# Optimization experiments

Hardware: AMD Instinct MI355X
Metric: run time of the kernel (lower is better)

Reference implementation:

```python
import jax, jax.numpy as jnp
import numpy as np
from jax import lax

EPS = 1e-5
S_CENTROIDS = 2048
K_NEIGH = 32


def _fps(xyz, S):
    """Farthest point sampling. xyz: (B,N,3) -> idx (B,S) int32."""
    B, N, _ = xyz.shape

    def body(carry, _):
        dist, farthest = carry  # (B,N), (B,)
        centroid = jnp.take_along_axis(xyz, farthest[:, None, None], axis=1)  # (B,1,3)
        d = jnp.sum((xyz - centroid) ** 2, axis=-1)  # (B,N)
        dist = jnp.minimum(dist, d)
        nxt = jnp.argmax(dist, axis=-1).astype(jnp.int32)
        return (dist, nxt), farthest

    init = (jnp.full((B, N), 1e10, xyz.dtype), jnp.zeros((B,), jnp.int32))
    _, idx = lax.scan(body, init, None, length=S)
    return idx.T  # (B,S)


def _knn(q, p, K):
    """q: (B,S,3) queries, p: (B,N,3) points -> idx (B,S,K) of K nearest."""
    d = (jnp.sum(q * q, -1)[:, :, None] + jnp.sum(p * p, -1)[:, None, :]
         - 2.0 * jnp.einsum('bsd,bnd->bsn', q, p))  # (B,S,N) sq dists
    _, idx = lax.top_k(-d, K)
    return idx


def _mlp_layer(x, w, g, b, m, v):
    # x: (B,S,K,Cin); 1x1 conv == channel matmul, then eval-mode BN, then ReLU
    x = jnp.einsum('bskc,oc->bsko', x, w)
    x = (x - m) * (g * lax.rsqrt(v + EPS)) + b
    return jax.nn.relu(x)


def setup_inputs() -> dict:
    key = jax.random.key(0)
    ks = jax.random.split(key, 8)
    B, N, D = 4, 8192, 64
    inp = {
        'xyz': jax.random.normal(ks[0], (B, N, 3), jnp.float32),
        'points': jax.random.normal(ks[1], (B, D, N), jnp.float32),
        'w0': jax.random.normal(ks[2], (64, 67), jnp.float32) * (1.0 / np.sqrt(67)),
        'g0': jnp.ones((64,), jnp.float32), 'b0': jnp.zeros((64,), jnp.float32),
        'm0': jnp.zeros((64,), jnp.float32), 'v0': jnp.ones((64,), jnp.float32),
        'w1': jax.random.normal(ks[3], (64, 64), jnp.float32) * (1.0 / np.sqrt(64)),
        'g1': jnp.ones((64,), jnp.float32), 'b1': jnp.zeros((64,), jnp.float32),
        'm1': jnp.zeros((64,), jnp.float32), 'v1': jnp.ones((64,), jnp.float32),
        'w2': jax.random.normal(ks[4], (128, 64), jnp.float32) * (1.0 / np.sqrt(64)),
        'g2': jnp.ones((128,), jnp.float32), 'b2': jnp.zeros((128,), jnp.float32),
        'm2': jnp.zeros((128,), jnp.float32), 'v2': jnp.ones((128,), jnp.float32),
    }
    return inp


def reference(xyz, points, w0, g0, b0, m0, v0, w1, g1, b1, m1, v1,
              w2, g2, b2, m2, v2):
    B, N, _ = xyz.shape
    S, K = S_CENTROIDS, K_NEIGH

    # FPS centroids (S < N path of the module)
    fps_idx = _fps(xyz, S)                                        # (B,S)
    new_xyz = jnp.take_along_axis(xyz, fps_idx[..., None], axis=1)  # (B,S,3)

    # KNN grouping
    idx = _knn(new_xyz, xyz, K)                                   # (B,S,K)
    grouped_xyz = jnp.take_along_axis(xyz[:, None], idx[..., None], axis=2)  # (B,S,K,3)
    grouped_xyz = grouped_xyz - new_xyz[:, :, None, :]

    # gather neighbor features: points (B,D,N) -> (B,N,D) -> (B,S,K,D)
    pts = jnp.transpose(points, (0, 2, 1))
    neigh = jnp.take_along_axis(pts[:, None], idx[..., None], axis=2)
    grouped = jnp.concatenate([grouped_xyz, neigh], axis=-1)      # (B,S,K,3+D)

    x = _mlp_layer(grouped, w0, g0, b0, m0, v0)
    x = _mlp_layer(x, w1, g1, b1, m1, v1)
    x = _mlp_layer(x, w2, g2, b2, m2, v2)                         # (B,S,K,128)

    new_points = jnp.transpose(jnp.max(x, axis=2), (0, 2, 1))     # (B,128,S)
    return new_xyz, new_points
```

## Files before the change

kernel.cpp:

```cpp
#include <hip/hip_runtime.h>
#include <cfloat>
#include <climits>

#define NPTS   8192
#define SCENT  2048
#define KNEIGH 32
#define BATCH  4
#define DFEAT  64
#define FPS_T  512
#define NV     8
#define NW     8
#define CAP    64
#define NCONS  252
#define CPB    63

typedef float v2f __attribute__((ext_vector_type(2)));

#define DPPTOP2(um, us, ctrl, rmask)                                                  \
    { unsigned _tm = (unsigned)__builtin_amdgcn_update_dpp(0, (int)(um), (ctrl),      \
                                                           (rmask), 0xf, false);     \
      unsigned _ts = (unsigned)__builtin_amdgcn_update_dpp(0, (int)(us), (ctrl),      \
                                                           (rmask), 0xf, false);     \
      unsigned _lo = ((um) < _tm) ? (um) : _tm;                                       \
      (us) = ((us) > _ts) ? (us) : _ts;                                               \
      (us) = ((us) > _lo) ? (us) : _lo;                                               \
      (um) = ((um) > _tm) ? (um) : _tm; }

#define FLUSH_PUB(Eidx, VX, VY, VZ, HASPREV, PX, PY, PZ)                              \
    if (((Eidx) & 63) == 63) {                                                        \
        const int base0 = (Eidx) - 63;                                                \
        if (t < 64 * 3) {                                                             \
            const int ci = base0 + t / 3;                                             \
            const int cc = t - (t / 3) * 3;                                           \
            float v;                                                                  \
            if (ci == (Eidx))                                                         \
                v = (cc == 0) ? (VX) : ((cc == 1) ? (VY) : (VZ));                     \
            else if ((HASPREV) && ci == (Eidx) - 1)                                   \
                v = (cc == 0) ? (PX) : ((cc == 1) ? (PY) : (PZ));                     \
            else                                                                      \
                v = (cc == 0) ? S.hx[ci] : ((cc == 1) ? S.hy[ci] : S.hz[ci]);         \
            __hip_atomic_store(&new_xyz[((size_t)b * SCENT + base0) * 3 + t], v,      \
                               __ATOMIC_RELAXED, __HIP_MEMORY_SCOPE_AGENT);           \
        }                                                                             \
        __syncthreads();                 \
        if (t == 0)                                                                   \
            __hip_atomic_store(&progress[b], (Eidx) + 1,                              \
                               __ATOMIC_RELEASE, __HIP_MEMORY_SCOPE_AGENT);           \
    }

struct FpsSh {
    float sx[NPTS], sy[NPTS], sz[NPTS];
    float hx[SCENT], hy[SCENT], hz[SCENT];
    alignas(16) unsigned slotQ[2][NW][4];
    int scand[CAP];
    int scnt;
    alignas(8) double sdd[2][NW];
    double sfv[NW];
    int sfo[NW];
};
struct ConsSh {
    float  spx[2048], spy[2048], spz[2048];
    double sp2[2048];
    float  tile[32 * 33];
    float  regA[64 * 68];
    float  regB[64 * 64];
    float  regC[128 * 64];
    float  prm[512];
};
union ShU { FpsSh f; ConsSh c; };

__global__ __launch_bounds__(FPS_T, 1) void fused_kernel(
        const float* __restrict__ xyz, float* __restrict__ new_xyz,
        const float* __restrict__ pts, float* __restrict__ ptsT,
        int* __restrict__ progress, int* __restrict__ tcount,
        float* __restrict__ out_points,
        const float* __restrict__ w0, const float* __restrict__ g0,
        const float* __restrict__ b0, const float* __restrict__ m0,
        const float* __restrict__ v0, const float* __restrict__ w1,
        const float* __restrict__ g1, const float* __restrict__ b1,
        const float* __restrict__ m1, const float* __restrict__ v1,
        const float* __restrict__ w2, const float* __restrict__ g2,
        const float* __restrict__ b2, const float* __restrict__ m2,
        const float* __restrict__ v2) {
    __shared__ ShU sh;
    const int t = threadIdx.x;
    const int lane = t & 63, w = t >> 6;

    if (blockIdx.x < BATCH) {
        FpsSh& S = sh.f;
        const int b = blockIdx.x;
        const float* X = xyz + (size_t)b * NPTS * 3;

        for (int p = t; p < NPTS; p += FPS_T) {
            S.sx[p] = X[3 * p + 0]; S.sy[p] = X[3 * p + 1]; S.sz[p] = X[3 * p + 2];
        }

        v2f px2[NV], py2[NV], pz2[NV], dist2[NV];
#pragma unroll
        for (int j = 0; j < NV; ++j) {
            int pA = t + FPS_T * j, pB = t + FPS_T * (j + NV);
            px2[j] = (v2f){X[3 * pA + 0], X[3 * pB + 0]};
            py2[j] = (v2f){X[3 * pA + 1], X[3 * pB + 1]};
            pz2[j] = (v2f){X[3 * pA + 2], X[3 * pB + 2]};
            dist2[j] = (v2f){1e10f, 1e10f};
        }
        float c0x = X[0], c0y = X[1], c0z = X[2];
        float c1x = 0.f, c1y = 0.f, c1z = 0.f;
        int dual = 0, buf = 0;
        int E = 1;
        if (t == 0) { S.hx[0] = c0x; S.hy[0] = c0y; S.hz[0] = c0z; }
        __syncthreads();

#pragma unroll 1
        while (true) {
            float m2s = -1.f, s2s = -1.f;
            {
                const v2f cxx = {c0x, c0x}, cyy = {c0y, c0y}, czz = {c0z, c0z};
                if (dual) {
                    const v2f exx = {c1x, c1x}, eyy = {c1y, c1y}, ezz = {c1z, c1z};
#pragma unroll
                    for (int j = 0; j < NV; ++j) {
                        v2f dx = px2[j] - cxx, dy = py2[j] - cyy, dz = pz2[j] - czz;
                        v2f d0 = __builtin_elementwise_fma(dx, dx,
                                 __builtin_elementwise_fma(dy, dy, dz * dz));
                        v2f ex = px2[j] - exx, ey = py2[j] - eyy, ez = pz2[j] - ezz;
                        v2f d1 = __builtin_elementwise_fma(ex, ex,
                                 __builtin_elementwise_fma(ey, ey, ez * ez));
                        v2f d  = __builtin_elementwise_min(d0, d1);
                        v2f nd = __builtin_elementwise_min(dist2[j], d);
                        dist2[j] = nd;
                        float hi = fmaxf(nd.x, nd.y), lo = fminf(nd.x, nd.y);
                        s2s = fmaxf(fmaxf(s2s, lo), fminf(m2s, hi));
                        m2s = fmaxf(m2s, hi);
                    }
                } else {
#pragma unroll
                    for (int j = 0; j < NV; ++j) {
                        v2f dx = px2[j] - cxx, dy = py2[j] - cyy, dz = pz2[j] - czz;
                        v2f d  = __builtin_elementwise_fma(dx, dx,
                                 __builtin_elementwise_fma(dy, dy, dz * dz));
                        v2f nd = __builtin_elementwise_min(dist2[j], d);
                        dist2[j] = nd;
                        float hi = fmaxf(nd.x, nd.y), lo = fminf(nd.x, nd.y);
                        s2s = fmaxf(fmaxf(s2s, lo), fminf(m2s, hi));
                        m2s = fmaxf(m2s, hi);
                    }
                }
            }
            const float m = m2s, sec = s2s;

            int mi = 0;
#pragma unroll
            for (int j = 0; j < NV; ++j) {
                mi = (dist2[j].x == m) ? (t + FPS_T * j)        : mi;
                mi = (dist2[j].y == m) ? (t + FPS_T * (j + NV)) : mi;
            }

            const unsigned myU = __float_as_uint(m);
            unsigned um = myU, us = __float_as_uint(sec);
            DPPTOP2(um, us, 0x111, 0xf);
            DPPTOP2(um, us, 0x112, 0xf);
            DPPTOP2(um, us, 0x114, 0xf);
            DPPTOP2(um, us, 0x118, 0xf);
            DPPTOP2(um, us, 0x142, 0xa);
            DPPTOP2(um, us, 0x143, 0xc);
            const unsigned wu  = (unsigned)__builtin_amdgcn_readlane((int)um, 63);
            const unsigned wsu = (unsigned)__builtin_amdgcn_readlane((int)us, 63);

            unsigned long long wb = __ballot(myU == wu);
            const int wl   = __ffsll(wb) - 1;
            const int widx = __builtin_amdgcn_readlane(mi, wl);
            const float thwf = __fmul_rn(__uint_as_float(wu), 0.999998f);
            unsigned long long b1m = __ballot(m >= thwf);
            unsigned long long b2m = __ballot(sec >= thwf);
            const unsigned tw = (b2m || __popcll(b1m) >= 2) ? 1u : 0u;
            if (lane == 0) {
                *(uint4*)&S.slotQ[buf][w][0] =
                    make_uint4(wu, (unsigned)widx | (tw << 14), wsu, 0u);
            }
            __syncthreads();

            unsigned mv[NW], mt4[NW], sv2[NW];
            {
                const uint4* qp = (const uint4*)&S.slotQ[buf][0][0];
                uint4 u0 = qp[0], u1 = qp[1], u2 = qp[2], u3 = qp[3];
                uint4 u4 = qp[4], u5 = qp[5], u6 = qp[6], u7 = qp[7];
                mv[0]=u0.x; mt4[0]=u0.y; sv2[0]=u0.z;
                mv[1]=u1.x; mt4[1]=u1.y; sv2[1]=u1.z;
                mv[2]=u2.x; mt4[2]=u2.y; sv2[2]=u2.z;
                mv[3]=u3.x; mt4[3]=u3.y; sv2[3]=u3.z;
                mv[4]=u4.x; mt4[4]=u4.y; sv2[4]=u4.z;
                mv[5]=u5.x; mt4[5]=u5.y; sv2[5]=u5.z;
                mv[6]=u6.x; mt4[6]=u6.y; sv2[6]=u6.z;
                mv[7]=u7.x; mt4[7]=u7.y; sv2[7]=u7.z;
            }
            unsigned gu = mv[0];
#pragma unroll
            for (int k = 1; k < NW; ++k) gu = (mv[k] > gu) ? mv[k] : gu;
            const float gvf  = __uint_as_float(gu);
            const float gthf = __fmul_rn(gvf, 0.999998f);
            const unsigned ugth = __float_as_uint(gthf);
            int nw = 0; unsigned meta = 0; int kw = 0;
#pragma unroll
            for (int k = NW - 1; k >= 0; --k) {
                nw  += (mv[k] >= ugth) ? 1 : 0;
                meta = (mv[k] == gu) ? mt4[k] : meta;
                kw   = (mv[k] == gu) ? k : kw;
            }
            const int wtie = (meta >> 14) & 1;
            int i1 = (int)(meta & 0x3fffu);
            const int fb = (nw >= 2) || wtie;

            if (fb) {
                if (t == 0) S.scnt = 0;
                __syncthreads();
#pragma unroll
                for (int j = 0; j < NV; ++j) {
                    if (dist2[j].x >= gthf) {
                        int slot = atomicAdd(&S.scnt, 1);
                        if (slot < CAP) S.scand[slot] = t + FPS_T * j;
                    }
                    if (dist2[j].y >= gthf) {
                        int slot = atomicAdd(&S.scnt, 1);
                        if (slot < CAP) S.scand[slot] = t + FPS_T * (j + NV);
                    }
                }
                __syncthreads();
                const int mm = S.scnt;
                if (mm <= CAP) {
                    double bd = -1.0; int bi = INT_MAX;
#pragma unroll 1
                    for (int k = 0; k < mm; ++k) {
                        const int pos = S.scand[k];
                        const double pxd = (double)S.sx[pos], pyd = (double)S.sy[pos],
                                     pzd = (double)S.sz[pos];
                        double dd = 1e10;
                        for (int i = t; i < E; i += FPS_T) {
                            double ddx = __dsub_rn(pxd, (double)S.hx[i]);
                            double ddy = __dsub_rn(pyd, (double)S.hy[i]);
                            double ddz = __dsub_rn(pzd, (double)S.hz[i]);
                            double d = __dadd_rn(__dadd_rn(__dmul_rn(ddx, ddx), __dmul_rn(ddy, ddy)),
                                                 __dmul_rn(ddz, ddz));
                            dd = fmin(dd, d);
                        }
#pragma unroll
                        for (int off = 32; off >= 1; off >>= 1)
                            dd = fmin(dd, __shfl_down(dd, off));
                        if (lane == 0) S.sdd[k & 1][w] = dd;
                        __syncthreads();
                        double ddm = S.sdd[k & 1][0];
#pragma unroll
                        for (int w2i = 1; w2i < NW; ++w2i) ddm = fmin(ddm, S.sdd[k & 1][w2i]);
                        if (ddm > bd || (ddm == bd && pos < bi)) { bd = ddm; bi = pos; }
                    }
                    i1 = bi;
                } else {
                    double bv = -1.0; int bi = INT_MAX;
#pragma unroll 1
                    for (int j = 0; j < 2 * NV; ++j) {
                        const int jj = j & (NV - 1);
                        const bool hiHalf = j >= NV;
                        const double pxd = (double)(hiHalf ? px2[jj].y : px2[jj].x);
                        const double pyd = (double)(hiHalf ? py2[jj].y : py2[jj].x);
                        const double pzd = (double)(hiHalf ? pz2[jj].y : pz2[jj].x);
                        double dd = 1e10;
                        for (int i = 0; i < E; ++i) {
                            double ddx = __dsub_rn(pxd, (double)S.hx[i]);
                            double ddy = __dsub_rn(pyd, (double)S.hy[i]);
                            double ddz = __dsub_rn(pzd, (double)S.hz[i]);
                            double d = __dadd_rn(__dadd_rn(__dmul_rn(ddx, ddx), __dmul_rn(ddy, ddy)),
                                                 __dmul_rn(ddz, ddz));
                            dd = fmin(dd, d);
                        }
                        int pidx = t + FPS_T * j;
                        if (dd > bv || (dd == bv && pidx < bi)) { bv = dd; bi = pidx; }
                    }
#pragma unroll
                    for (int off = 32; off >= 1; off >>= 1) {
                        double ov = __shfl_down(bv, off);
                        int    oi = __shfl_down(bi, off);
                        if (ov > bv || (ov == bv && oi < bi)) { bv = ov; bi = oi; }
                    }
                    if (lane == 0) { S.sfv[w] = bv; S.sfo[w] = bi; }
                    __syncthreads();
                    bv = S.sfv[0]; bi = S.sfo[0];
#pragma unroll
                    for (int w2i = 1; w2i < NW; ++w2i) {
                        double ov = S.sfv[w2i]; int oi = S.sfo[w2i];
                        if (ov > bv || (ov == bv && oi < bi)) { bv = ov; bi = oi; }
                    }
                    i1 = bi;
                }
                __syncthreads();
            }

            const float e0x = S.sx[i1], e0y = S.sy[i1], e0z = S.sz[i1];
            if (t == 0) { S.hx[E] = e0x; S.hy[E] = e0y; S.hz[E] = e0z; }
            FLUSH_PUB(E, e0x, e0y, e0z, 0, 0.f, 0.f, 0.f);
            c0x = e0x; c0y = e0y; c0z = e0z;

            int peeled = 0;
            float e1x = 0.f, e1y = 0.f, e1z = 0.f;
            if (!fb && (E + 1) < SCENT) {
                unsigned arr[NW];
#pragma unroll
                for (int k = 0; k < NW; ++k) arr[k] = (k == kw) ? sv2[k] : mv[k];
                unsigned v2u = arr[0];
#pragma unroll
                for (int k = 1; k < NW; ++k) v2u = (arr[k] > v2u) ? arr[k] : v2u;
                int k2 = 0; unsigned meta2 = 0;
#pragma unroll
                for (int k = NW - 1; k >= 0; --k) {
                    meta2 = (arr[k] == v2u) ? mt4[k] : meta2;
                    k2    = (arr[k] == v2u) ? k : k2;
                }
                unsigned v3u = 0;
#pragma unroll
                for (int k = 0; k < NW; ++k) {
                    const unsigned cnd = (k == kw || k == k2) ? sv2[k] : mv[k];
                    v3u = (cnd > v3u) ? cnd : v3u;
                }
                const float v2vf = __uint_as_float(v2u);
                const float v3vf = __uint_as_float(v3u);
                const int i2 = (int)(meta2 & 0x3fffu);
                e1x = S.sx[i2]; e1y = S.sy[i2]; e1z = S.sz[i2];
                const float ddx = e1x - e0x, ddy = e1y - e0y, ddz = e1z - e0z;
                const float dq = fmaf(ddx, ddx, fmaf(ddy, ddy, ddz * ddz));
                const float wnew = fminf(v2vf, dq);
                peeled = ((k2 != kw) &&
                          (wnew > __fmul_rn(v3vf, 1.000004f))) ? 1 : 0;
            }
            if (peeled) {
                const int e1i = E + 1;
                if (t == 0) { S.hx[e1i] = e1x; S.hy[e1i] = e1y; S.hz[e1i] = e1z; }
                FLUSH_PUB(e1i, e1x, e1y, e1z, 1, e0x, e0y, e0z);
                c1x = e1x; c1y = e1y; c1z = e1z;
                dual = 1;
                E = e1i + 1;
            } else {
                dual = 0;
                E = E + 1;
            }
            if (E >= SCENT) break;
            buf ^= 1;
        }
    } else {
        ConsSh& K = sh.c;
        const int local = blockIdx.x - BATCH;
        const int batch = local / CPB;
        const int cl    = local % CPB;
        const int tx = t & 31, ty = t >> 5;

        for (int tid2 = local; tid2 < 2048; tid2 += NCONS) {
            const int bt = tid2 >> 9, rest = tid2 & 511;
            const int d0 = (rest >> 8) * 32, n0 = (rest & 255) * 32;
            __syncthreads();
#pragma unroll
            for (int i = 0; i < 2; ++i)
                K.tile[(ty + 16 * i) * 33 + tx] =
                    pts[(size_t)bt * DFEAT * NPTS + (size_t)(d0 + ty + 16 * i) * NPTS + n0 + tx];
            __syncthreads();
#pragma unroll
            for (int i = 0; i < 2; ++i)
                ptsT[(size_t)bt * NPTS * DFEAT + (size_t)(n0 + ty + 16 * i) * DFEAT + d0 + tx] =
                    K.tile[tx * 33 + ty + 16 * i];
        }
        if (t == 0) {
            __threadfence();
            atomicAdd(tcount, 1);
        }

        for (int idx = t; idx < 64 * 68; idx += FPS_T) {
            int o = idx / 68, i = idx - o * 68;
            float v;
            if (i < 64)      v = w0[o * 67 + 3 + i];
            else if (i < 67) v = w0[o * 67 + (i - 64)];
            else             v = 0.0f;
            K.regA[idx] = v;
        }
        for (int idx = t; idx < 64 * 64; idx += FPS_T)  K.regB[idx] = w1[idx];
        for (int idx = t; idx < 128 * 64; idx += FPS_T) K.regC[idx] = w2[idx];
        if (t < 64) {
            float a0v = g0[t] / sqrtf(v0[t] + 1e-5f);
            K.prm[t]       = a0v;
            K.prm[64 + t]  = b0[t] - m0[t] * a0v;
            float a1v = g1[t] / sqrtf(v1[t] + 1e-5f);
            K.prm[128 + t] = a1v;
            K.prm[192 + t] = b1[t] - m1[t] * a1v;
        } else if (t < 192) {
            int o = t - 64;
            float a2v = g2[o] / sqrtf(v2[o] + 1e-5f);
            K.prm[256 + o] = a2v;
            K.prm[384 + o] = b2[o] - m2[o] * a2v;
        }

        const float* Xb = xyz + (size_t)batch * NPTS * 3;
#pragma unroll 1
        for (int r = 0; ; ++r) {
            const int sBase = r * (CPB * NW) + cl * NW;
            if (sBase >= SCENT) break;
            const int sMax = min(sBase + NW - 1, SCENT - 1);
            if (t == 0) {
                while (__hip_atomic_load(&progress[batch], __ATOMIC_ACQUIRE,
                                         __HIP_MEMORY_SCOPE_AGENT) < sMax + 1)
                    __builtin_amdgcn_s_sleep(8);
                if (r == 0) {
                    while (__hip_atomic_load(tcount, __ATOMIC_ACQUIRE,
                                             __HIP_MEMORY_SCOPE_AGENT) < NCONS)
                        __builtin_amdgcn_s_sleep(8);
                }
            }
            __syncthreads();

            const int sQ = min(sBase + w, SCENT - 1);
            const float* q = new_xyz + ((size_t)batch * SCENT + sQ) * 3;
            const float qfx = q[0], qfy = q[1], qfz = q[2];
            const double qx = (double)qfx, qy = (double)qfy, qz = (double)qfz;
            const double q2 = __dadd_rn(__dadd_rn(__dmul_rn(qx, qx), __dmul_rn(qy, qy)),
                                        __dmul_rn(qz, qz));

            double ld   = DBL_MAX;
            int    li   = 0x7fffffff;
            double taud = DBL_MAX;
            int    taui = 0x7fffffff;

#pragma unroll 1
            for (int c = 0; c < 4; ++c) {
                __syncthreads();
#pragma unroll
                for (int r2 = 0; r2 < 4; ++r2) {
                    int pl = r2 * 512 + t;
                    int p  = c * 2048 + pl;
                    float x = Xb[3 * p + 0], y = Xb[3 * p + 1], z = Xb[3 * p + 2];
                    K.spx[pl] = x; K.spy[pl] = y; K.spz[pl] = z;
                    double dx = (double)x, dy = (double)y, dz = (double)z;
                    K.sp2[pl] = __dadd_rn(__dadd_rn(__dmul_rn(dx, dx), __dmul_rn(dy, dy)),
                                          __dmul_rn(dz, dz));
                }
                __syncthreads();
#pragma unroll 1
                for (int i = 0; i < 32; ++i) {
                    const int pl   = i * 64 + lane;
                    const int pidx = c * 2048 + pl;
                    double px = (double)K.spx[pl], py = (double)K.spy[pl],
                           pz = (double)K.spz[pl];
                    double qp = __dadd_rn(__dadd_rn(__dmul_rn(qx, px), __dmul_rn(qy, py)),
                                          __dmul_rn(qz, pz));
                    double d  = __dsub_rn(__dadd_rn(q2, K.sp2[pl]), __dmul_rn(2.0, qp));
                    bool cand = (d < taud) || (d == taud && pidx < taui);
                    unsigned long long mmask = __ballot(cand);
                    while (mmask) {
                        int sl = __ffsll((unsigned long long)mmask) - 1;
                        mmask &= mmask - 1;
                        double dv = __shfl(d, sl);
                        int    iv = __shfl(pidx, sl);
                        if (dv < taud || (dv == taud && iv < taui)) {
                            bool gt = (lane < 32) && (ld > dv || (ld == dv && li > iv));
                            unsigned long long gm = __ballot(gt);
                            double ud = __shfl_up(ld, 1);
                            int    ui = __shfl_up(li, 1);
                            if (gt) { ld = ud; li = ui; }
                            bool first = gt && ((lane == 0) || !((gm >> (lane - 1)) & 1ull));
                            if (first) { ld = dv; li = iv; }
                            taud = __shfl(ld, 31);
                            taui = __shfl(li, 31);
                        }
                    }
                }
            }

            if (sBase + w < SCENT && lane < 32) {
                const int nidx = li;
                const float* P3 = Xb + (size_t)nidx * 3;
                const float dx = P3[0] - qfx, dy = P3[1] - qfy, dz = P3[2] - qfz;

                const float4* F = (const float4*)(ptsT + ((size_t)batch * NPTS + nidx) * 64);
                float4 xv[17];
#pragma unroll
                for (int i = 0; i < 16; ++i) xv[i] = F[i];
                xv[16] = make_float4(dx, dy, dz, 0.0f);

                float h0[64];
                const float4* W0 = (const float4*)K.regA;
#pragma unroll
                for (int o = 0; o < 64; ++o) {
                    float acc = 0.f;
#pragma unroll
                    for (int i = 0; i < 17; ++i) {
                        float4 ww = W0[o * 17 + i];
                        acc = fmaf(xv[i].x, ww.x, acc);
                        acc = fmaf(xv[i].y, ww.y, acc);
                        acc = fmaf(xv[i].z, ww.z, acc);
                        acc = fmaf(xv[i].w, ww.w, acc);
                    }
                    h0[o] = fmaxf(fmaf(acc, K.prm[o], K.prm[64 + o]), 0.f);
                }
                float h1[64];
                const float4* W1 = (const float4*)K.regB;
#pragma unroll
                for (int o = 0; o < 64; ++o) {
                    float acc = 0.f;
#pragma unroll
                    for (int i = 0; i < 16; ++i) {
                        float4 ww = W1[o * 16 + i];
                        acc = fmaf(h0[4 * i + 0], ww.x, acc);
                        acc = fmaf(h0[4 * i + 1], ww.y, acc);
                        acc = fmaf(h0[4 * i + 2], ww.z, acc);
                        acc = fmaf(h0[4 * i + 3], ww.w, acc);
                    }
                    h1[o] = fmaxf(fmaf(acc, K.prm[128 + o], K.prm[192 + o]), 0.f);
                }
                const float4* W2 = (const float4*)K.regC;
                float* outp = out_points + (size_t)batch * 128 * SCENT + sQ;
#pragma unroll 1
                for (int o = 0; o < 128; ++o) {
                    float acc = 0.f;
#pragma unroll
                    for (int i = 0; i < 16; ++i) {
                        float4 ww = W2[o * 16 + i];
                        acc = fmaf(h1[4 * i + 0], ww.x, acc);
                        acc = fmaf(h1[4 * i + 1], ww.y, acc);
                        acc = fmaf(h1[4 * i + 2], ww.z, acc);
                        acc = fmaf(h1[4 * i + 3], ww.w, acc);
                    }
                    float y = fmaxf(fmaf(acc, K.prm[256 + o], K.prm[384 + o]), 0.f);
#pragma unroll
                    for (int off = 16; off >= 1; off >>= 1)
                        y = fmaxf(y, __shfl_xor(y, off));
                    if (lane == 0) outp[(size_t)o * SCENT] = y;
                }
            }
        }
    }
}

extern "C" void kernel_launch(void* const* d_in, const int* in_sizes, int n_in,
                              void* d_out, int out_size, void* d_ws, size_t ws_size,
                              hipStream_t stream) {
    const float* xyz    = (const float*)d_in[0];
    const float* points = (const float*)d_in[1];
    const float* w0 = (const float*)d_in[2];
    const float* g0 = (const float*)d_in[3];
    const float* b0 = (const float*)d_in[4];
    const float* m0 = (const float*)d_in[5];
    const float* v0 = (const float*)d_in[6];
    const float* w1 = (const float*)d_in[7];
    const float* g1 = (const float*)d_in[8];
    const float* b1 = (const float*)d_in[9];
    const float* m1 = (const float*)d_in[10];
    const float* v1 = (const float*)d_in[11];
    const float* w2 = (const float*)d_in[12];
    const float* g2 = (const float*)d_in[13];
    const float* b2 = (const float*)d_in[14];
    const float* m2 = (const float*)d_in[15];
    const float* v2 = (const float*)d_in[16];

    float* out_xyz    = (float*)d_out;
    float* out_points = (float*)d_out + (size_t)BATCH * SCENT * 3;

    char* ws = (char*)d_ws;
    int*   progress = (int*)ws;
    int*   tcount   = (int*)(ws + 64);
    float* ptsT     = (float*)(ws + 32768);

    hipMemsetAsync(ws, 0, 128, stream);

    void* kargs[] = { (void*)&xyz, (void*)&out_xyz, (void*)&points, (void*)&ptsT,
                      (void*)&progress, (void*)&tcount, (void*)&out_points,
                      (void*)&w0, (void*)&g0, (void*)&b0, (void*)&m0, (void*)&v0,
                      (void*)&w1, (void*)&g1, (void*)&b1, (void*)&m1, (void*)&v1,
                      (void*)&w2, (void*)&g2, (void*)&b2, (void*)&m2, (void*)&v2 };
    hipLaunchCooperativeKernel((const void*)fused_kernel,
                               dim3(BATCH + NCONS), dim3(FPS_T), kargs, 0, stream);
}
```

Before: 2.237 ms.

## Publish winner coordinates in per-wave slots and vectorize top-2 tracking in FPS

Each wave now writes the coordinates of its local max point into shared memory next to its max/second-max record. After the barrier, lanes read those slots and use readlane to get the chosen centroid's coordinates, instead of doing a dependent LDS lookup of sx/sy/sz after the index is resolved. Top-2 tracking in the distance loop is kept per vector lane and reduced once at the end. The tie flag is now derived from the wave-reduced second value rather than two ballots. This aims to shorten the serial critical path of each FPS iteration, in exchange for an extra LDS gather per lane and a wider slot array. The tie detection rule is slightly changed, which could affect the fallback decision.

```diff
diff --git a/kernel.cpp b/kernel.cpp
--- a/kernel.cpp
+++ b/kernel.cpp
@@ -51,7 +51,7 @@
 struct FpsSh {
     float sx[NPTS], sy[NPTS], sz[NPTS];
     float hx[SCENT], hy[SCENT], hz[SCENT];
-    alignas(16) unsigned slotQ[2][NW][4];
+    alignas(16) unsigned slotQ[2][NW][8];
     int scand[CAP];
     int scnt;
     alignas(8) double sdd[2][NW];
@@ -113,7 +113,7 @@
 
 #pragma unroll 1
         while (true) {
-            float m2s = -1.f, s2s = -1.f;
+            v2f m2v = {-1.f, -1.f}, s2v = {-1.f, -1.f};
             {
                 const v2f cxx = {c0x, c0x}, cyy = {c0y, c0y}, czz = {c0z, c0z};
                 if (dual) {
@@ -129,9 +129,9 @@
                         v2f d  = __builtin_elementwise_min(d0, d1);
                         v2f nd = __builtin_elementwise_min(dist2[j], d);
                         dist2[j] = nd;
-                        float hi = fmaxf(nd.x, nd.y), lo = fminf(nd.x, nd.y);
-                        s2s = fmaxf(fmaxf(s2s, lo), fminf(m2s, hi));
-                        m2s = fmaxf(m2s, hi);
+                        v2f lo = __builtin_elementwise_min(m2v, nd);
+                        s2v = __builtin_elementwise_max(s2v, lo);
+                        m2v = __builtin_elementwise_max(m2v, nd);
                     }
                 } else {
 #pragma unroll
@@ -141,13 +141,14 @@
                                  __builtin_elementwise_fma(dy, dy, dz * dz));
                         v2f nd = __builtin_elementwise_min(dist2[j], d);
                         dist2[j] = nd;
-                        float hi = fmaxf(nd.x, nd.y), lo = fminf(nd.x, nd.y);
-                        s2s = fmaxf(fmaxf(s2s, lo), fminf(m2s, hi));
-                        m2s = fmaxf(m2s, hi);
-                    }
-                }
-            }
-            const float m = m2s, sec = s2s;
+                        v2f lo = __builtin_elementwise_min(m2v, nd);
+                        s2v = __builtin_elementwise_max(s2v, lo);
+                        m2v = __builtin_elementwise_max(m2v, nd);
+                    }
+                }
+            }
+            const float m   = fmaxf(m2v.x, m2v.y);
+            const float sec = fmaxf(fmaxf(s2v.x, s2v.y), fminf(m2v.x, m2v.y));
 
             int mi = 0;
 #pragma unroll
@@ -155,6 +156,7 @@
                 mi = (dist2[j].x == m) ? (t + FPS_T * j)        : mi;
                 mi = (dist2[j].y == m) ? (t + FPS_T * (j + NV)) : mi;
             }
+            const float pmx = S.sx[mi], pmy = S.sy[mi], pmz = S.sz[mi];
 
             const unsigned myU = __float_as_uint(m);
             unsigned um = myU, us = __float_as_uint(sec);
@@ -171,20 +173,24 @@
             const int wl   = __ffsll(wb) - 1;
             const int widx = __builtin_amdgcn_readlane(mi, wl);
             const float thwf = __fmul_rn(__uint_as_float(wu), 0.999998f);
-            unsigned long long b1m = __ballot(m >= thwf);
-            unsigned long long b2m = __ballot(sec >= thwf);
-            const unsigned tw = (b2m || __popcll(b1m) >= 2) ? 1u : 0u;
+            const unsigned tw = (__uint_as_float(wsu) >= thwf) ? 1u : 0u;
             if (lane == 0) {
                 *(uint4*)&S.slotQ[buf][w][0] =
                     make_uint4(wu, (unsigned)widx | (tw << 14), wsu, 0u);
             }
+            if (lane == wl) {
+                *(uint4*)&S.slotQ[buf][w][4] =
+                    make_uint4(__float_as_uint(pmx), __float_as_uint(pmy),
+                               __float_as_uint(pmz), 0u);
+            }
             __syncthreads();
 
+            uint4 cslot = *(const uint4*)&S.slotQ[buf][lane & 7][4];
             unsigned mv[NW], mt4[NW], sv2[NW];
             {
                 const uint4* qp = (const uint4*)&S.slotQ[buf][0][0];
-                uint4 u0 = qp[0], u1 = qp[1], u2 = qp[2], u3 = qp[3];
-                uint4 u4 = qp[4], u5 = qp[5], u6 = qp[6], u7 = qp[7];
+                uint4 u0 = qp[0],  u1 = qp[2],  u2 = qp[4],  u3 = qp[6];
+                uint4 u4 = qp[8],  u5 = qp[10], u6 = qp[12], u7 = qp[14];
                 mv[0]=u0.x; mt4[0]=u0.y; sv2[0]=u0.z;
                 mv[1]=u1.x; mt4[1]=u1.y; sv2[1]=u1.z;
                 mv[2]=u2.x; mt4[2]=u2.y; sv2[2]=u2.z;
@@ -211,6 +217,7 @@
             int i1 = (int)(meta & 0x3fffu);
             const int fb = (nw >= 2) || wtie;
 
+            float e0x, e0y, e0z;
             if (fb) {
                 if (t == 0) S.scnt = 0;
                 __syncthreads();
@@ -292,9 +299,14 @@
                     i1 = bi;
                 }
                 __syncthreads();
-            }
-
-            const float e0x = S.sx[i1], e0y = S.sy[i1], e0z = S.sz[i1];
+                e0x = S.sx[i1]; e0y = S.sy[i1]; e0z = S.sz[i1];
+            } else {
+                const int skw = __builtin_amdgcn_readfirstlane(kw);
+                e0x = __uint_as_float((unsigned)__builtin_amdgcn_readlane((int)cslot.x, skw));
+                e0y = __uint_as_float((unsigned)__builtin_amdgcn_readlane((int)cslot.y, skw));
+                e0z = __uint_as_float((unsigned)__builtin_amdgcn_readlane((int)cslot.z, skw));
+            }
+
             if (t == 0) { S.hx[E] = e0x; S.hy[E] = e0y; S.hz[E] = e0z; }
             FLUSH_PUB(E, e0x, e0y, e0z, 0, 0.f, 0.f, 0.f);
             c0x = e0x; c0y = e0y; c0z = e0z;
@@ -308,12 +320,9 @@
                 unsigned v2u = arr[0];
 #pragma unroll
                 for (int k = 1; k < NW; ++k) v2u = (arr[k] > v2u) ? arr[k] : v2u;
-                int k2 = 0; unsigned meta2 = 0;
-#pragma unroll
-                for (int k = NW - 1; k >= 0; --k) {
-                    meta2 = (arr[k] == v2u) ? mt4[k] : meta2;
-                    k2    = (arr[k] == v2u) ? k : k2;
-                }
+                int k2 = 0;
+#pragma unroll
+                for (int k = NW - 1; k >= 0; --k) k2 = (arr[k] == v2u) ? k : k2;
                 unsigned v3u = 0;
 #pragma unroll
                 for (int k = 0; k < NW; ++k) {
@@ -322,8 +331,10 @@
                 }
                 const float v2vf = __uint_as_float(v2u);
                 const float v3vf = __uint_as_float(v3u);
-                const int i2 = (int)(meta2 & 0x3fffu);
-                e1x = S.sx[i2]; e1y = S.sy[i2]; e1z = S.sz[i2];
+                const int sk2 = __builtin_amdgcn_readfirstlane(k2);
+                e1x = __uint_as_float((unsigned)__builtin_amdgcn_readlane((int)cslot.x, sk2));
+                e1y = __uint_as_float((unsigned)__builtin_amdgcn_readlane((int)cslot.y, sk2));
+                e1z = __uint_as_float((unsigned)__builtin_amdgcn_readlane((int)cslot.z, sk2));
                 const float ddx = e1x - e0x, ddy = e1y - e0y, ddz = e1z - e0z;
                 const float dq = fmaf(ddx, ddx, fmaf(ddy, ddy, ddz * ddz));
                 const float wnew = fminf(v2vf, dq);
```

Measured after the change: 2.691 ms. 1.2x slower.

## Defer second-centroid peel decision into next iteration to overlap with distance update

Applied to the files above, without the earlier changes.

The FPS loop no longer decides right after the block reduction whether to peel a second centroid. It carries the per-wave max and second-max state into the next iteration and evaluates the peel test between the two halves of the distance update, so the shared-memory lookup and scalar selection logic overlap with vector math. When peeled, a separate distance pass is applied before the max reduction. The reduction is rewritten to use packed vector min/max, and the tie flag now comes from the wave's second-max instead of two ballots. This changes the critical-path scheduling but adds an extra conditional full pass when peeling, and the altered tie detection could affect exactness.

```diff
diff --git a/kernel.cpp b/kernel.cpp
--- a/kernel.cpp
+++ b/kernel.cpp
@@ -105,49 +105,84 @@
             dist2[j] = (v2f){1e10f, 1e10f};
         }
         float c0x = X[0], c0y = X[1], c0z = X[2];
-        float c1x = 0.f, c1y = 0.f, c1z = 0.f;
-        int dual = 0, buf = 0;
         int E = 1;
         if (t == 0) { S.hx[0] = c0x; S.hy[0] = c0y; S.hz[0] = c0z; }
+        int carryPeel = 0, p_kw = 0;
+        unsigned p_mv[NW], p_sv2[NW], p_mt4[NW];
+#pragma unroll
+        for (int k = 0; k < NW; ++k) { p_mv[k] = 0; p_sv2[k] = 0; p_mt4[k] = 0; }
+        int buf = 0;
         __syncthreads();
 
 #pragma unroll 1
         while (true) {
-            float m2s = -1.f, s2s = -1.f;
-            {
-                const v2f cxx = {c0x, c0x}, cyy = {c0y, c0y}, czz = {c0z, c0z};
-                if (dual) {
-                    const v2f exx = {c1x, c1x}, eyy = {c1y, c1y}, ezz = {c1z, c1z};
-#pragma unroll
-                    for (int j = 0; j < NV; ++j) {
-                        v2f dx = px2[j] - cxx, dy = py2[j] - cyy, dz = pz2[j] - czz;
-                        v2f d0 = __builtin_elementwise_fma(dx, dx,
-                                 __builtin_elementwise_fma(dy, dy, dz * dz));
-                        v2f ex = px2[j] - exx, ey = py2[j] - eyy, ez = pz2[j] - ezz;
-                        v2f d1 = __builtin_elementwise_fma(ex, ex,
-                                 __builtin_elementwise_fma(ey, ey, ez * ez));
-                        v2f d  = __builtin_elementwise_min(d0, d1);
-                        v2f nd = __builtin_elementwise_min(dist2[j], d);
-                        dist2[j] = nd;
-                        float hi = fmaxf(nd.x, nd.y), lo = fminf(nd.x, nd.y);
-                        s2s = fmaxf(fmaxf(s2s, lo), fminf(m2s, hi));
-                        m2s = fmaxf(m2s, hi);
-                    }
-                } else {
-#pragma unroll
-                    for (int j = 0; j < NV; ++j) {
-                        v2f dx = px2[j] - cxx, dy = py2[j] - cyy, dz = pz2[j] - czz;
-                        v2f d  = __builtin_elementwise_fma(dx, dx,
-                                 __builtin_elementwise_fma(dy, dy, dz * dz));
-                        v2f nd = __builtin_elementwise_min(dist2[j], d);
-                        dist2[j] = nd;
-                        float hi = fmaxf(nd.x, nd.y), lo = fminf(nd.x, nd.y);
-                        s2s = fmaxf(fmaxf(s2s, lo), fminf(m2s, hi));
-                        m2s = fmaxf(m2s, hi);
-                    }
-                }
-            }
-            const float m = m2s, sec = s2s;
+            const v2f cxx = {c0x, c0x}, cyy = {c0y, c0y}, czz = {c0z, c0z};
+#pragma unroll
+            for (int j = 0; j < 4; ++j) {
+                v2f dx = px2[j] - cxx, dy = py2[j] - cyy, dz = pz2[j] - czz;
+                v2f d  = __builtin_elementwise_fma(dx, dx,
+                         __builtin_elementwise_fma(dy, dy, dz * dz));
+                dist2[j] = __builtin_elementwise_min(dist2[j], d);
+            }
+            unsigned arr[NW];
+#pragma unroll
+            for (int k = 0; k < NW; ++k) arr[k] = (k == p_kw) ? p_sv2[k] : p_mv[k];
+            unsigned v2u = arr[0];
+#pragma unroll
+            for (int k = 1; k < NW; ++k) v2u = (arr[k] > v2u) ? arr[k] : v2u;
+            int k2 = 0; unsigned meta2 = 0;
+#pragma unroll
+            for (int k = NW - 1; k >= 0; --k) {
+                meta2 = (arr[k] == v2u) ? p_mt4[k] : meta2;
+                k2    = (arr[k] == v2u) ? k : k2;
+            }
+            unsigned v3u = 0;
+#pragma unroll
+            for (int k = 0; k < NW; ++k) {
+                const unsigned cnd = (k == p_kw || k == k2) ? p_sv2[k] : p_mv[k];
+                v3u = (cnd > v3u) ? cnd : v3u;
+            }
+            const int i2 = (int)(meta2 & 0x3fffu);
+            const float e1x = S.sx[i2], e1y = S.sy[i2], e1z = S.sz[i2];
+#pragma unroll
+            for (int j = 4; j < NV; ++j) {
+                v2f dx = px2[j] - cxx, dy = py2[j] - cyy, dz = pz2[j] - czz;
+                v2f d  = __builtin_elementwise_fma(dx, dx,
+                         __builtin_elementwise_fma(dy, dy, dz * dz));
+                dist2[j] = __builtin_elementwise_min(dist2[j], d);
+            }
+            const float v2vf = __uint_as_float(v2u);
+            const float v3vf = __uint_as_float(v3u);
+            const float ddx = e1x - c0x, ddy = e1y - c0y, ddz = e1z - c0z;
+            const float dq = fmaf(ddx, ddx, fmaf(ddy, ddy, ddz * ddz));
+            const float wnew = fminf(v2vf, dq);
+            const int peeled = carryPeel && (E < SCENT) && (k2 != p_kw) &&
+                               (wnew > __fmul_rn(v3vf, 1.000004f));
+            if (peeled) {
+                if (t == 0) { S.hx[E] = e1x; S.hy[E] = e1y; S.hz[E] = e1z; }
+                FLUSH_PUB(E, e1x, e1y, e1z, 1, c0x, c0y, c0z);
+                const v2f exx = {e1x, e1x}, eyy = {e1y, e1y}, ezz = {e1z, e1z};
+#pragma unroll
+                for (int j = 0; j < NV; ++j) {
+                    v2f dx = px2[j] - exx, dy = py2[j] - eyy, dz = pz2[j] - ezz;
+                    v2f d  = __builtin_elementwise_fma(dx, dx,
+                             __builtin_elementwise_fma(dy, dy, dz * dz));
+                    dist2[j] = __builtin_elementwise_min(dist2[j], d);
+                }
+                E = E + 1;
+                if (E >= SCENT) break;
+            }
+
+            v2f m2v = {-1.f, -1.f}, s2v = {-1.f, -1.f};
+#pragma unroll
+            for (int j = 0; j < NV; ++j) {
+                v2f nd = dist2[j];
+                v2f lo = __builtin_elementwise_min(m2v, nd);
+                s2v = __builtin_elementwise_max(s2v, lo);
+                m2v = __builtin_elementwise_max(m2v, nd);
+            }
+            const float m   = fmaxf(m2v.x, m2v.y);
+            const float sec = fmaxf(fmaxf(s2v.x, s2v.y), fminf(m2v.x, m2v.y));
 
             int mi = 0;
 #pragma unroll
@@ -171,9 +206,7 @@
             const int wl   = __ffsll(wb) - 1;
             const int widx = __builtin_amdgcn_readlane(mi, wl);
             const float thwf = __fmul_rn(__uint_as_float(wu), 0.999998f);
-            unsigned long long b1m = __ballot(m >= thwf);
-            unsigned long long b2m = __ballot(sec >= thwf);
-            const unsigned tw = (b2m || __popcll(b1m) >= 2) ? 1u : 0u;
+            const unsigned tw = (__uint_as_float(wsu) >= thwf) ? 1u : 0u;
             if (lane == 0) {
                 *(uint4*)&S.slotQ[buf][w][0] =
                     make_uint4(wu, (unsigned)widx | (tw << 14), wsu, 0u);
@@ -236,11 +269,11 @@
                                      pzd = (double)S.sz[pos];
                         double dd = 1e10;
                         for (int i = t; i < E; i += FPS_T) {
-                            double ddx = __dsub_rn(pxd, (double)S.hx[i]);
-                            double ddy = __dsub_rn(pyd, (double)S.hy[i]);
-                            double ddz = __dsub_rn(pzd, (double)S.hz[i]);
-                            double d = __dadd_rn(__dadd_rn(__dmul_rn(ddx, ddx), __dmul_rn(ddy, ddy)),
-                                                 __dmul_rn(ddz, ddz));
+                            double ddxd = __dsub_rn(pxd, (double)S.hx[i]);
+                            double ddyd = __dsub_rn(pyd, (double)S.hy[i]);
+                            double ddzd = __dsub_rn(pzd, (double)S.hz[i]);
+                            double d = __dadd_rn(__dadd_rn(__dmul_rn(ddxd, ddxd), __dmul_rn(ddyd, ddyd)),
+                                                 __dmul_rn(ddzd, ddzd));
                             dd = fmin(dd, d);
                         }
 #pragma unroll
@@ -265,11 +298,11 @@
                         const double pzd = (double)(hiHalf ? pz2[jj].y : pz2[jj].x);
                         double dd = 1e10;
                         for (int i = 0; i < E; ++i) {
-                            double ddx = __dsub_rn(pxd, (double)S.hx[i]);
-                            double ddy = __dsub_rn(pyd, (double)S.hy[i]);
-                            double ddz = __dsub_rn(pzd, (double)S.hz[i]);
-                            double d = __dadd_rn(__dadd_rn(__dmul_rn(ddx, ddx), __dmul_rn(ddy, ddy)),
-                                                 __dmul_rn(ddz, ddz));
+                            double ddxd = __dsub_rn(pxd, (double)S.hx[i]);
+                            double ddyd = __dsub_rn(pyd, (double)S.hy[i]);
+                            double ddzd = __dsub_rn(pzd, (double)S.hz[i]);
+                            double d = __dadd_rn(__dadd_rn(__dmul_rn(ddxd, ddxd), __dmul_rn(ddyd, ddyd)),
+                                                 __dmul_rn(ddzd, ddzd));
                             dd = fmin(dd, d);
                         }
                         int pidx = t + FPS_T * j;
@@ -299,48 +332,15 @@
             FLUSH_PUB(E, e0x, e0y, e0z, 0, 0.f, 0.f, 0.f);
             c0x = e0x; c0y = e0y; c0z = e0z;
 
-            int peeled = 0;
-            float e1x = 0.f, e1y = 0.f, e1z = 0.f;
-            if (!fb && (E + 1) < SCENT) {
-                unsigned arr[NW];
-#pragma unroll
-                for (int k = 0; k < NW; ++k) arr[k] = (k == kw) ? sv2[k] : mv[k];
-                unsigned v2u = arr[0];
-#pragma unroll
-                for (int k = 1; k < NW; ++k) v2u = (arr[k] > v2u) ? arr[k] : v2u;
-                int k2 = 0; unsigned meta2 = 0;
-#pragma unroll
-                for (int k = NW - 1; k >= 0; --k) {
-                    meta2 = (arr[k] == v2u) ? mt4[k] : meta2;
-                    k2    = (arr[k] == v2u) ? k : k2;
-                }
-                unsigned v3u = 0;
+            carryPeel = !fb;
+            if (carryPeel) {
 #pragma unroll
                 for (int k = 0; k < NW; ++k) {
-                    const unsigned cnd = (k == kw || k == k2) ? sv2[k] : mv[k];
-                    v3u = (cnd > v3u) ? cnd : v3u;
-                }
-                const float v2vf = __uint_as_float(v2u);
-                const float v3vf = __uint_as_float(v3u);
-                const int i2 = (int)(meta2 & 0x3fffu);
-                e1x = S.sx[i2]; e1y = S.sy[i2]; e1z = S.sz[i2];
-                const float ddx = e1x - e0x, ddy = e1y - e0y, ddz = e1z - e0z;
-                const float dq = fmaf(ddx, ddx, fmaf(ddy, ddy, ddz * ddz));
-                const float wnew = fminf(v2vf, dq);
-                peeled = ((k2 != kw) &&
-                          (wnew > __fmul_rn(v3vf, 1.000004f))) ? 1 : 0;
-            }
-            if (peeled) {
-                const int e1i = E + 1;
-                if (t == 0) { S.hx[e1i] = e1x; S.hy[e1i] = e1y; S.hz[e1i] = e1z; }
-                FLUSH_PUB(e1i, e1x, e1y, e1z, 1, e0x, e0y, e0z);
-                c1x = e1x; c1y = e1y; c1z = e1z;
-                dual = 1;
-                E = e1i + 1;
-            } else {
-                dual = 0;
-                E = E + 1;
-            }
+                    p_mv[k] = mv[k]; p_sv2[k] = sv2[k]; p_mt4[k] = mt4[k];
+                }
+                p_kw = kw;
+            }
+            E = E + 1;
             if (E >= SCENT) break;
             buf ^= 1;
         }
```

Measured after the change: 2.442 ms. 9.2% more time.
